# Kernel optimization log

Hardware: AMD Instinct MI355X
Metric: run time of the kernel (lower is better)

The kernel has to match this reference:

```python
import jax, jax.numpy as jnp
import numpy as np

P = 2        # patch size (all 3 dims)
NB = 8       # num_bands
N = 16       # d_state
DTR = 8      # dt_rank = d_model // 16
DCONV = 4    # d_conv
SMAX = 2.0   # smax_dt = smax_B = smax_C


def _ln(x, g, b):
    mu = x.mean(-1, keepdims=True)
    v = ((x - mu) ** 2).mean(-1, keepdims=True)
    return (x - mu) / jnp.sqrt(v + 1e-5) * g + b


def _silu(x):
    return x * jax.nn.sigmoid(x)


def _ssm_layer(x, band, m, rho, Win, bin_, convw, convb, Wx, Wdt, bdt, Alog, Dp,
               Wout, bout, edt, eB, eC, wr, wm):
    # x: [B, L, d_model] -> bidirectional conditioned selective scan (BiFCSSM)
    Bsz, L, _ = x.shape
    ED = convw.shape[0]
    xz = x @ Win + bin_
    xp, z = xz[..., :ED], xz[..., ED:]
    # depthwise causal conv1d over L
    xpad = jnp.pad(xp, ((0, 0), (DCONV - 1, 0), (0, 0)))
    xc = sum(xpad[:, k:k + L, :] * convw[:, k] for k in range(DCONV)) + convb
    xc = _silu(xc)
    dbl = xc @ Wx                                    # [B,L,DTR+2N]
    dt = jax.nn.softplus(dbl[..., :DTR] @ Wdt + bdt)  # [B,L,ED]
    # band/radius/mask conditioned modulation of delta, B, C
    s_dt = SMAX * jax.nn.sigmoid(edt[band][None] + wr[0] * rho[None] + wm[0] * m)
    s_B = SMAX * jax.nn.sigmoid(eB[band][None] + wr[1] * rho[None] + wm[1] * m)
    s_C = SMAX * jax.nn.sigmoid(eC[band][None] + wr[2] * rho[None] + wm[2] * m)
    dt = dt * s_dt[..., None]
    Bm = dbl[..., DTR:DTR + N] * s_B[..., None]       # [B,L,N]
    Cm = dbl[..., DTR + N:] * s_C[..., None]          # [B,L,N]
    A = -jnp.exp(Alog)                                # [ED,N]
    dA = jnp.exp(dt[..., None] * A)                   # [B,L,ED,N]
    dBu = (dA - 1.0) / A * Bm[:, :, None, :] * xc[..., None]   # exact ZOH
    dA_s = jnp.moveaxis(dA, 1, 0)
    dBu_s = jnp.moveaxis(dBu, 1, 0)
    C_s = jnp.moveaxis(Cm, 1, 0)
    h0 = jnp.zeros((Bsz, ED, N), x.dtype)

    def step(h, inp):
        a, bu, c = inp
        h = a * h + bu
        return h, jnp.einsum('ben,bn->be', h, c)

    _, yf = jax.lax.scan(step, h0, (dA_s, dBu_s, C_s))
    _, yb = jax.lax.scan(step, h0, (dA_s, dBu_s, C_s), reverse=True)
    y = jnp.moveaxis(yf + yb, 0, 1) + Dp * xc
    y = y * _silu(z)
    return y @ Wout + bout


def _fwd(kspace_ri, mask, pe_w, pe_b, pu_w, pu_b, ln_g, ln_b, fn_g, fn_b,
         cond_band, cond_rad_w, cond_mask_w, l0_Win, l0_bin, l0_convw, l0_convb,
         l0_Wx, l0_Wdt, l0_bdt, l0_Alog, l0_D, l0_Wout, l0_bout, l0_edt, l0_eB,
         l0_eC, l0_wr, l0_wm):
    Bsz, C, nx, ny, nz = kspace_ri.shape
    gx, gy, gz = nx // P, ny // P, nz // P
    L = gx * gy * gz
    # patch embed (Conv3d, kernel==stride) as blocked einsum
    xr = kspace_ri.reshape(Bsz, C, gx, P, gy, P, gz, P)
    x = jnp.einsum('bcxiyjzk,dcijk->bdxyz', xr, pe_w) + pe_b[None, :, None, None, None]
    DM = x.shape[1]
    x = x.reshape(Bsz, DM, L).transpose(0, 2, 1)               # [B,L,D]
    m = mask.reshape(Bsz, 1, gx, P, gy, P, gz, P).mean(axis=(3, 5, 7)).reshape(Bsz, L)
    m = jnp.clip(m, 0.0, 1.0)
    # raster scan ordering: identity permutation, rho_bar, band ids
    rho = jnp.arange(L, dtype=x.dtype) / float(L - 1)
    band = jnp.clip(jnp.floor(rho * NB).astype(jnp.int32), 0, NB - 1)
    # condition tokens
    cond = cond_band[band][None] + rho[None, :, None] * cond_rad_w + m[:, :, None] * cond_mask_w
    h = _ln(x + cond, ln_g, ln_b)
    h = h + _ssm_layer(_ln(h, fn_g, fn_b), band, m, rho, l0_Win, l0_bin, l0_convw,
                       l0_convb, l0_Wx, l0_Wdt, l0_bdt, l0_Alog, l0_D, l0_Wout,
                       l0_bout, l0_edt, l0_eB, l0_eC, l0_wr, l0_wm)
    # patch unembed (ConvTranspose3d, kernel==stride) as blocked einsum
    hg = h.transpose(0, 2, 1).reshape(Bsz, DM, gx, gy, gz)
    out = jnp.einsum('bdxyz,dcijk->bcxiyjzk', hg, pu_w).reshape(Bsz, C, nx, ny, nz)
    out = out + pu_b[None, :, None, None, None]
    return kspace_ri + out


def setup_inputs() -> dict:
    key = jax.random.key(0)
    ks = jax.random.split(key, 24)
    ED, DM, CIN = 256, 128, 16

    def nrm(k, shape, s):
        return jax.random.normal(k, shape, jnp.float32) * s

    return {
        'kspace_ri': jax.random.normal(ks[0], (1, CIN, 64, 64, 16), jnp.float32),
        'mask': jax.random.uniform(ks[1], (1, 1, 64, 64, 16), jnp.float32),
        'pe_w': nrm(ks[2], (DM, CIN, P, P, P), 0.09),
        'pe_b': nrm(ks[3], (DM,), 0.02),
        'pu_w': nrm(ks[4], (DM, CIN, P, P, P), 0.05),
        'pu_b': jnp.zeros((CIN,), jnp.float32),
        'ln_g': jnp.ones((DM,), jnp.float32),
        'ln_b': jnp.zeros((DM,), jnp.float32),
        'fn_g': jnp.ones((DM,), jnp.float32),
        'fn_b': jnp.zeros((DM,), jnp.float32),
        'cond_band': nrm(ks[5], (NB, DM), 0.02),
        'cond_rad_w': nrm(ks[6], (DM,), 0.02),
        'cond_mask_w': nrm(ks[7], (DM,), 0.02),
        'l0_Win': nrm(ks[8], (DM, 2 * ED), 0.05),
        'l0_bin': jnp.zeros((2 * ED,), jnp.float32),
        'l0_convw': nrm(ks[9], (ED, DCONV), 0.2),
        'l0_convb': jnp.zeros((ED,), jnp.float32),
        'l0_Wx': nrm(ks[10], (ED, DTR + 2 * N), 0.05),
        'l0_Wdt': nrm(ks[11], (DTR, ED), 0.1),
        'l0_bdt': jnp.full((ED,), -3.0, jnp.float32),
        'l0_Alog': jnp.log(jnp.tile(jnp.arange(1, N + 1, dtype=jnp.float32), (ED, 1))),
        'l0_D': jnp.ones((ED,), jnp.float32),
        'l0_Wout': nrm(ks[12], (ED, DM), 0.05),
        'l0_bout': jnp.zeros((DM,), jnp.float32),
        'l0_edt': nrm(ks[13], (NB,), 0.1),
        'l0_eB': nrm(ks[14], (NB,), 0.1),
        'l0_eC': nrm(ks[15], (NB,), 0.1),
        'l0_wr': nrm(ks[16], (3,), 0.1),
        'l0_wm': nrm(ks[17], (3,), 0.1),
    }


def reference(kspace_ri, mask, pe_w, pe_b, pu_w, pu_b, ln_g, ln_b, fn_g, fn_b,
              cond_band, cond_rad_w, cond_mask_w, l0_Win, l0_bin, l0_convw,
              l0_convb, l0_Wx, l0_Wdt, l0_bdt, l0_Alog, l0_D, l0_Wout, l0_bout,
              l0_edt, l0_eB, l0_eC, l0_wr, l0_wm):
    return _fwd(kspace_ri, mask, pe_w, pe_b, pu_w, pu_b, ln_g, ln_b, fn_g, fn_b,
                cond_band, cond_rad_w, cond_mask_w, l0_Win, l0_bin, l0_convw,
                l0_convb, l0_Wx, l0_Wdt, l0_bdt, l0_Alog, l0_D, l0_Wout, l0_bout,
                l0_edt, l0_eB, l0_eC, l0_wr, l0_wm)
```

## Files before the change

kernel.cpp:

```cpp
#include <hip/hip_runtime.h>
#include <hip/hip_bf16.h>

#define L_TOK 8192
#define NCh 256
#define CLh 32
#define LOG2E 1.44269504088896f

typedef short bf16x8 __attribute__((ext_vector_type(8)));
typedef float f32x4 __attribute__((ext_vector_type(4)));

static __device__ __forceinline__ float nexp2(float x) {
#if __has_builtin(__builtin_amdgcn_exp2f)
    return __builtin_amdgcn_exp2f(x);
#else
    return exp2f(x);
#endif
}
static __device__ __forceinline__ float sigm(float x) {
    return 1.f / (1.f + nexp2(-x * LOG2E));
}

static __device__ __forceinline__ ushort f2bf(float x) {
    union { float f; uint u; } v; v.f = x;
    uint r = v.u + 0x7fffu + ((v.u >> 16) & 1u);
    return (ushort)(r >> 16);
}
static __device__ __forceinline__ float bf2f(ushort h) {
    union { float f; uint u; } v; v.u = ((uint)h) << 16;
    return v.f;
}
static __device__ __forceinline__ void f2hl(float x, ushort* hi, ushort* lo) {
    ushort h = f2bf(x);
    *hi = h;
    *lo = f2bf(x - bf2f(h));
}

#define W_PE   0
#define W_WIN  16384
#define W_WOUT 81920
#define W_PU   114688
#define W_PROJ 131072
#define W_TOT  212992

__global__ __launch_bounds__(256) void prep_k(const float* __restrict__ pe_w, const float* __restrict__ Win,
                                              const float* __restrict__ Wx, const float* __restrict__ Wdt,
                                              const float* __restrict__ Wout, const float* __restrict__ pu_w,
                                              const float* __restrict__ mask,
                                              ushort* __restrict__ wH, ushort* __restrict__ wL,
                                              float* __restrict__ mbuf) {
    int b = blockIdx.x;
    if (b >= 832) {
        int l = (b - 832) * 256 + threadIdx.x;
        int xg = l >> 8, yg = (l >> 3) & 31, zg = l & 7;
        float s = 0.f;
        for (int i2 = 0; i2 < 2; ++i2)
            for (int j2 = 0; j2 < 2; ++j2)
                for (int k2 = 0; k2 < 2; ++k2)
                    s += mask[(2 * xg + i2) * 1024 + (2 * yg + j2) * 16 + 2 * zg + k2];
        s *= 0.125f;
        mbuf[l] = fminf(fmaxf(s, 0.f), 1.f);
        return;
    }
    int i = b * 256 + threadIdx.x;
    float v;
    if (i < 16384) {
        v = pe_w[i];
    } else if (i < 81920) {
        int j = i - 16384; int n = j >> 7, k = j & 127;
        v = Win[k * 512 + n];
    } else if (i < 114688) {
        int j = i - 81920; int n = j >> 8, k = j & 255;
        v = Wout[k * 128 + n];
    } else if (i < 131072) {
        int j = i - 114688; int n = j >> 7, k = j & 127;
        v = pu_w[k * 128 + n];
    } else {
        int j = i - 131072; int n = j >> 8, k = j & 255;
        if (n < 256) {
            float s = 0.f;
#pragma unroll
            for (int r = 0; r < 8; ++r) s += Wx[k * 40 + r] * Wdt[r * 256 + n];
            v = s;
        } else if (n < 288) {
            v = Wx[k * 40 + 8 + (n - 256)];
        } else {
            v = 0.f;
        }
    }
    ushort h, lo; f2hl(v, &h, &lo);
    wH[i] = h; wL[i] = lo;
}

__global__ __launch_bounds__(256) void embed_ln_k(const float* __restrict__ ks,
                                                  const ushort* __restrict__ wH, const ushort* __restrict__ wL,
                                                  const float* __restrict__ pe_b, const float* __restrict__ cond_band,
                                                  const float* __restrict__ cond_rad, const float* __restrict__ cond_mask,
                                                  const float* __restrict__ mbuf,
                                                  const float* __restrict__ ln_g, const float* __restrict__ ln_b,
                                                  const float* __restrict__ fn_g, const float* __restrict__ fn_b,
                                                  float* __restrict__ h_,
                                                  ushort* __restrict__ hnH, ushort* __restrict__ hnL) {
    __shared__ __align__(16) char smem[41472];
    ushort (*AsH)[72] = (ushort(*)[72])(smem);
    ushort (*AsL)[72] = (ushort(*)[72])(smem + 2304);
    ushort (*BsH)[72] = (ushort(*)[72])(smem + 4608);
    ushort (*BsL)[72] = (ushort(*)[72])(smem + 23040);
    float  (*Cs)[132] = (float(*)[132])(smem);

    const int tid = threadIdx.x;
    const int lane = tid & 63, wn = tid >> 6;
    const int ln = lane & 15, q = lane >> 4;
    const int mb = blockIdx.x * 16;

    f32x4 acc[2];
    acc[0] = (f32x4){0.f, 0.f, 0.f, 0.f};
    acc[1] = (f32x4){0.f, 0.f, 0.f, 0.f};

    for (int kc = 0; kc < 128; kc += 64) {
        __syncthreads();
        for (int u = tid; u < 1024; u += 256) {
            int r = u >> 6, kk = u & 63;
            int l = mb + r, k = kc + kk;
            int cc = k >> 3, ijk = k & 7;
            int xg = l >> 8, yg = (l >> 3) & 31, zg = l & 7;
            int i2 = (ijk >> 2) & 1, j2 = (ijk >> 1) & 1, k2 = ijk & 1;
            float v = ks[cc * 65536 + (2 * xg + i2) * 1024 + (2 * yg + j2) * 16 + 2 * zg + k2];
            ushort h, lo; f2hl(v, &h, &lo);
            AsH[r][kk] = h; AsL[r][kk] = lo;
        }
        for (int u = tid; u < 1024; u += 256) {
            int n = u >> 3, g = u & 7;
            *(uint4*)&BsH[n][g * 8] = *(const uint4*)&wH[W_PE + n * 128 + kc + g * 8];
            *(uint4*)&BsL[n][g * 8] = *(const uint4*)&wL[W_PE + n * 128 + kc + g * 8];
        }
        __syncthreads();
#pragma unroll
        for (int ks_ = 0; ks_ < 64; ks_ += 32) {
            const int kk = ks_ + q * 8;
            bf16x8 ah = *(const bf16x8*)&AsH[ln][kk];
            bf16x8 al = *(const bf16x8*)&AsL[ln][kk];
#pragma unroll
            for (int cb = 0; cb < 2; ++cb) {
                bf16x8 bh = *(const bf16x8*)&BsH[wn * 32 + cb * 16 + ln][kk];
                bf16x8 bl = *(const bf16x8*)&BsL[wn * 32 + cb * 16 + ln][kk];
                acc[cb] = __builtin_amdgcn_mfma_f32_16x16x32_bf16(ah, bh, acc[cb], 0, 0, 0);
                acc[cb] = __builtin_amdgcn_mfma_f32_16x16x32_bf16(ah, bl, acc[cb], 0, 0, 0);
                acc[cb] = __builtin_amdgcn_mfma_f32_16x16x32_bf16(al, bh, acc[cb], 0, 0, 0);
            }
        }
    }
    __syncthreads();
#pragma unroll
    for (int cb = 0; cb < 2; ++cb) {
#pragma unroll
        for (int r = 0; r < 4; ++r) {
            int row = q * 4 + r;
            int col = wn * 32 + cb * 16 + ln;
            int l = mb + row;
            float rho = (float)l * (1.0f / 8191.0f);
            int band = min(7, (int)(rho * 8.0f));
            Cs[row][col] = acc[cb][r] + pe_b[col] + cond_band[band * 128 + col]
                           + rho * cond_rad[col] + mbuf[l] * cond_mask[col];
        }
    }
    __syncthreads();
    {
        int row = tid >> 4, j = tid & 15;
        int l = mb + row;
        float v8[8];
        float s = 0.f, s2 = 0.f;
#pragma unroll
        for (int i = 0; i < 8; ++i) {
            float v = Cs[row][j * 8 + i];
            v8[i] = v; s += v; s2 += v * v;
        }
#pragma unroll
        for (int o = 1; o < 16; o <<= 1) { s += __shfl_xor(s, o, 16); s2 += __shfl_xor(s2, o, 16); }
        float mu = s * (1.f / 128.f);
        float var = s2 * (1.f / 128.f) - mu * mu;
        float rstd = rsqrtf(fmaxf(var, 0.f) + 1e-5f);
        float hv[8];
        s = 0.f; s2 = 0.f;
#pragma unroll
        for (int i = 0; i < 8; ++i) {
            int col = j * 8 + i;
            float h = (v8[i] - mu) * rstd * ln_g[col] + ln_b[col];
            hv[i] = h; s += h; s2 += h * h;
        }
#pragma unroll
        for (int i = 0; i < 8; i += 4)
            *(float4*)&h_[(size_t)l * 128 + j * 8 + i] = make_float4(hv[i], hv[i + 1], hv[i + 2], hv[i + 3]);
#pragma unroll
        for (int o = 1; o < 16; o <<= 1) { s += __shfl_xor(s, o, 16); s2 += __shfl_xor(s2, o, 16); }
        mu = s * (1.f / 128.f);
        var = s2 * (1.f / 128.f) - mu * mu;
        rstd = rsqrtf(fmaxf(var, 0.f) + 1e-5f);
        union { ushort u[8]; uint4 v4; } oh, ol;
#pragma unroll
        for (int i = 0; i < 8; ++i) {
            int col = j * 8 + i;
            float o2 = (hv[i] - mu) * rstd * fn_g[col] + fn_b[col];
            ushort hh, ll; f2hl(o2, &hh, &ll);
            oh.u[i] = hh; ol.u[i] = ll;
        }
        *(uint4*)&hnH[(size_t)l * 128 + j * 8] = oh.v4;
        *(uint4*)&hnL[(size_t)l * 128 + j * 8] = ol.v4;
    }
}

__global__ __launch_bounds__(256) void win_k(const ushort* __restrict__ Ah, const ushort* __restrict__ Al,
                                             const ushort* __restrict__ wH, const ushort* __restrict__ wL,
                                             const float* __restrict__ bin_,
                                             float* __restrict__ xp, float* __restrict__ sz) {
    __shared__ ushort AsH[64][72], AsL[64][72];
    __shared__ ushort BsH[64][72], BsL[64][72];
    const int tid = threadIdx.x;
    const int lane = tid & 63, wave = tid >> 6;
    const int wm = wave & 1, wn = wave >> 1;
    const int ln = lane & 15, q = lane >> 4;
    const int mb = blockIdx.x * 64, nb = blockIdx.y * 64;

    f32x4 acc[2][2];
#pragma unroll
    for (int rb = 0; rb < 2; ++rb)
#pragma unroll
        for (int cb = 0; cb < 2; ++cb) acc[rb][cb] = (f32x4){0.f, 0.f, 0.f, 0.f};

    for (int kc = 0; kc < 128; kc += 64) {
        __syncthreads();
        for (int u = tid; u < 512; u += 256) {
            int r = u >> 3, g = u & 7;
            size_t go = (size_t)(mb + r) * 128 + kc + g * 8;
            *(uint4*)&AsH[r][g * 8] = *(const uint4*)&Ah[go];
            *(uint4*)&AsL[r][g * 8] = *(const uint4*)&Al[go];
        }
        for (int u = tid; u < 512; u += 256) {
            int n = u >> 3, g = u & 7;
            size_t go = (size_t)(W_WIN) + (size_t)(nb + n) * 128 + kc + g * 8;
            *(uint4*)&BsH[n][g * 8] = *(const uint4*)&wH[go];
            *(uint4*)&BsL[n][g * 8] = *(const uint4*)&wL[go];
        }
        __syncthreads();
#pragma unroll
        for (int ks_ = 0; ks_ < 64; ks_ += 32) {
            const int kk = ks_ + q * 8;
            bf16x8 ah[2], al[2], bh[2], bl[2];
#pragma unroll
            for (int rb = 0; rb < 2; ++rb) {
                ah[rb] = *(const bf16x8*)&AsH[wm * 32 + rb * 16 + ln][kk];
                al[rb] = *(const bf16x8*)&AsL[wm * 32 + rb * 16 + ln][kk];
            }
#pragma unroll
            for (int cb = 0; cb < 2; ++cb) {
                bh[cb] = *(const bf16x8*)&BsH[wn * 32 + cb * 16 + ln][kk];
                bl[cb] = *(const bf16x8*)&BsL[wn * 32 + cb * 16 + ln][kk];
            }
#pragma unroll
            for (int rb = 0; rb < 2; ++rb)
#pragma unroll
                for (int cb = 0; cb < 2; ++cb) {
                    acc[rb][cb] = __builtin_amdgcn_mfma_f32_16x16x32_bf16(ah[rb], bh[cb], acc[rb][cb], 0, 0, 0);
                    acc[rb][cb] = __builtin_amdgcn_mfma_f32_16x16x32_bf16(ah[rb], bl[cb], acc[rb][cb], 0, 0, 0);
                    acc[rb][cb] = __builtin_amdgcn_mfma_f32_16x16x32_bf16(al[rb], bh[cb], acc[rb][cb], 0, 0, 0);
                }
        }
    }
#pragma unroll
    for (int rb = 0; rb < 2; ++rb)
#pragma unroll
        for (int cb = 0; cb < 2; ++cb)
#pragma unroll
            for (int r = 0; r < 4; ++r) {
                int l = mb + wm * 32 + rb * 16 + q * 4 + r;
                int col = nb + wn * 32 + cb * 16 + ln;
                float v = acc[rb][cb][r] + bin_[col];
                if (col < 256) {
                    xp[(size_t)l * 256 + col] = v;
                } else {
                    sz[(size_t)l * 256 + (col - 256)] = v * sigm(v);
                }
            }
}

__global__ __launch_bounds__(256) void conv_k(const float* __restrict__ xp, const float* __restrict__ convw,
                                              const float* __restrict__ convb, float* __restrict__ xc) {
    int id = blockIdx.x * 256 + threadIdx.x;
    int l = id >> 6, e4 = (id & 63) * 4;
    float4 cw[4];
#pragma unroll
    for (int j = 0; j < 4; ++j) cw[j] = *(const float4*)&convw[(e4 + j) * 4];
    float4 cb = *(const float4*)&convb[e4];
    float o[4] = {cb.x, cb.y, cb.z, cb.w};
#pragma unroll
    for (int k = 0; k < 4; ++k) {
        int lp = l - 3 + k;
        if (lp >= 0) {
            float4 t = *(const float4*)&xp[(size_t)lp * 256 + e4];
            o[0] += t.x * ((const float*)&cw[0])[k];
            o[1] += t.y * ((const float*)&cw[1])[k];
            o[2] += t.z * ((const float*)&cw[2])[k];
            o[3] += t.w * ((const float*)&cw[3])[k];
        }
    }
    float4 r;
    r.x = o[0] * sigm(o[0]);
    r.y = o[1] * sigm(o[1]);
    r.z = o[2] * sigm(o[2]);
    r.w = o[3] * sigm(o[3]);
    *(float4*)&xc[(size_t)l * 256 + e4] = r;
}

__global__ __launch_bounds__(256) void proj_k(const float* __restrict__ xc,
                                              const ushort* __restrict__ wH, const ushort* __restrict__ wL,
                                              const float* __restrict__ bdt, const float* __restrict__ mbuf,
                                              const float* __restrict__ edt, const float* __restrict__ eB,
                                              const float* __restrict__ eC, const float* __restrict__ wr,
                                              const float* __restrict__ wm,
                                              float* __restrict__ dt, float* __restrict__ Bm, float* __restrict__ Cm) {
    __shared__ ushort AsH[64][72], AsL[64][72];
    __shared__ ushort BsH[64][72], BsL[64][72];
    const int tid = threadIdx.x;
    const int lane = tid & 63, wave = tid >> 6;
    const int wm_ = wave & 1, wn = wave >> 1;
    const int ln = lane & 15, q = lane >> 4;
    const int mb = blockIdx.x * 64, nb = blockIdx.y * 64;

    f32x4 acc[2][2];
#pragma unroll
    for (int rb = 0; rb < 2; ++rb)
#pragma unroll
        for (int cb = 0; cb < 2; ++cb) acc[rb][cb] = (f32x4){0.f, 0.f, 0.f, 0.f};

    for (int kc = 0; kc < 256; kc += 64) {
        __syncthreads();
        for (int u = tid; u < 1024; u += 256) {
            int r = u >> 4, kq = u & 15;
            float4 v = *(const float4*)&xc[(size_t)(mb + r) * 256 + kc + kq * 4];
            union { ushort u[4]; uint2 v2; } hh, ll;
            f2hl(v.x, &hh.u[0], &ll.u[0]); f2hl(v.y, &hh.u[1], &ll.u[1]);
            f2hl(v.z, &hh.u[2], &ll.u[2]); f2hl(v.w, &hh.u[3], &ll.u[3]);
            *(uint2*)&AsH[r][kq * 4] = hh.v2;
            *(uint2*)&AsL[r][kq * 4] = ll.v2;
        }
        for (int u = tid; u < 512; u += 256) {
            int n = u >> 3, g = u & 7;
            size_t go = (size_t)(W_PROJ) + (size_t)(nb + n) * 256 + kc + g * 8;
            *(uint4*)&BsH[n][g * 8] = *(const uint4*)&wH[go];
            *(uint4*)&BsL[n][g * 8] = *(const uint4*)&wL[go];
        }
        __syncthreads();
#pragma unroll
        for (int ks_ = 0; ks_ < 64; ks_ += 32) {
            const int kk = ks_ + q * 8;
            bf16x8 ah[2], al[2], bh[2], bl[2];
#pragma unroll
            for (int rb = 0; rb < 2; ++rb) {
                ah[rb] = *(const bf16x8*)&AsH[wm_ * 32 + rb * 16 + ln][kk];
                al[rb] = *(const bf16x8*)&AsL[wm_ * 32 + rb * 16 + ln][kk];
            }
#pragma unroll
            for (int cb = 0; cb < 2; ++cb) {
                bh[cb] = *(const bf16x8*)&BsH[wn * 32 + cb * 16 + ln][kk];
                bl[cb] = *(const bf16x8*)&BsL[wn * 32 + cb * 16 + ln][kk];
            }
#pragma unroll
            for (int rb = 0; rb < 2; ++rb)
#pragma unroll
                for (int cb = 0; cb < 2; ++cb) {
                    acc[rb][cb] = __builtin_amdgcn_mfma_f32_16x16x32_bf16(ah[rb], bh[cb], acc[rb][cb], 0, 0, 0);
                    acc[rb][cb] = __builtin_amdgcn_mfma_f32_16x16x32_bf16(ah[rb], bl[cb], acc[rb][cb], 0, 0, 0);
                    acc[rb][cb] = __builtin_amdgcn_mfma_f32_16x16x32_bf16(al[rb], bh[cb], acc[rb][cb], 0, 0, 0);
                }
        }
    }
#pragma unroll
    for (int rb = 0; rb < 2; ++rb)
#pragma unroll
        for (int cb = 0; cb < 2; ++cb)
#pragma unroll
            for (int r = 0; r < 4; ++r) {
                int l = mb + wm_ * 32 + rb * 16 + q * 4 + r;
                int col = nb + wn * 32 + cb * 16 + ln;
                float v = acc[rb][cb][r];
                float rho = (float)l * (1.0f / 8191.0f);
                int band = min(7, (int)(rho * 8.0f));
                float mv = mbuf[l];
                if (col < 256) {
                    float sc0 = 2.0f * sigm(edt[band] + wr[0] * rho + wm[0] * mv);
                    float v2 = v + bdt[col];
                    float sp = (v2 > 20.f) ? v2 : log1pf(expf(v2));
                    dt[(size_t)l * 256 + col] = sp * sc0;
                } else if (col < 272) {
                    float sc1 = 2.0f * sigm(eB[band] + wr[1] * rho + wm[1] * mv);
                    Bm[(size_t)l * 16 + (col - 256)] = v * sc1;
                } else if (col < 288) {
                    float sc2 = 2.0f * sigm(eC[band] + wr[2] * rho + wm[2] * mv);
                    Cm[(size_t)l * 16 + (col - 272)] = v * sc2;
                }
            }
}

template <int PHASE>
__global__ __launch_bounds__(256) void scan_k(const float* __restrict__ dt, const float* __restrict__ xc,
                                              const float* __restrict__ Bm, const float* __restrict__ Cm,
                                              const float* __restrict__ Alog,
                                              float* __restrict__ Hb, float* __restrict__ sdtb,
                                              float* __restrict__ yf, float* __restrict__ yb) {
    const int c = blockIdx.x, dir = blockIdx.y, e = threadIdx.x;
    __shared__ float bms[CLh][16];
    __shared__ float cms[CLh][16];
    for (int idx = e; idx < CLh * 16; idx += 256) {
        bms[idx >> 4][idx & 15] = Bm[c * (CLh * 16) + idx];
        if (PHASE == 1) cms[idx >> 4][idx & 15] = Cm[c * (CLh * 16) + idx];
    }
    float A2[16], iv[16], h[16];
#pragma unroll
    for (int n = 0; n < 16; ++n) {
        float ea = nexp2(Alog[e * 16 + n] * LOG2E);
        A2[n] = -ea * LOG2E;
        iv[n] = -1.0f / ea;
    }
    const size_t hofs = (size_t)(dir * NCh + c) * 4096 + e * 16;
    if (PHASE == 0) {
#pragma unroll
        for (int n = 0; n < 16; ++n) h[n] = 0.f;
    } else {
#pragma unroll
        for (int j = 0; j < 4; ++j) {
            float4 hv = *(const float4*)&Hb[hofs + 4 * j];
            h[4 * j] = hv.x; h[4 * j + 1] = hv.y; h[4 * j + 2] = hv.z; h[4 * j + 3] = hv.w;
        }
    }
    const int base = c * CLh;
    float cu[8], cx[8], nu[8], nx[8];
#pragma unroll
    for (int j = 0; j < 8; ++j) {
        int p = dir ? (CLh - 1 - j) : j;
        cu[j] = dt[(size_t)(base + p) * 256 + e];
        cx[j] = xc[(size_t)(base + p) * 256 + e];
    }
    __syncthreads();
    float sdt = 0.f;
    float* __restrict__ yp = dir ? yb : yf;
#pragma unroll
    for (int g = 0; g < CLh / 8; ++g) {
        if (g + 1 < CLh / 8) {
#pragma unroll
            for (int j = 0; j < 8; ++j) {
                int s = (g + 1) * 8 + j;
                int p = dir ? (CLh - 1 - s) : s;
                nu[j] = dt[(size_t)(base + p) * 256 + e];
                nx[j] = xc[(size_t)(base + p) * 256 + e];
            }
        }
#pragma unroll
        for (int j = 0; j < 8; ++j) {
            int s = g * 8 + j;
            int p = dir ? (CLh - 1 - s) : s;
            float u = cu[j], xv = cx[j];
            union { float4 v[4]; float f[16]; } bb, cc;
            const float4* bp = (const float4*)&bms[p][0];
            bb.v[0] = bp[0]; bb.v[1] = bp[1]; bb.v[2] = bp[2]; bb.v[3] = bp[3];
            if (PHASE == 1) {
                const float4* cp = (const float4*)&cms[p][0];
                cc.v[0] = cp[0]; cc.v[1] = cp[1]; cc.v[2] = cp[2]; cc.v[3] = cp[3];
            }
            float y = 0.f;
#pragma unroll
            for (int n = 0; n < 16; ++n) {
                float a = nexp2(A2[n] * u);
                float w = xv * bb.f[n] * iv[n];
                float t = h[n] + w;
                h[n] = a * t - w;
                if (PHASE == 1) y += h[n] * cc.f[n];
            }
            if (PHASE == 0) sdt += u;
            if (PHASE == 1) yp[(size_t)(base + p) * 256 + e] = y;
        }
#pragma unroll
        for (int j = 0; j < 8; ++j) { cu[j] = nu[j]; cx[j] = nx[j]; }
    }
    if (PHASE == 0) {
#pragma unroll
        for (int j = 0; j < 4; ++j) {
            float4 hv = make_float4(h[4 * j], h[4 * j + 1], h[4 * j + 2], h[4 * j + 3]);
            *(float4*)&Hb[hofs + 4 * j] = hv;
        }
        if (dir == 0) sdtb[c * 256 + e] = sdt;
    }
}

__global__ __launch_bounds__(64) void combine_k(const float* __restrict__ Hb, float* __restrict__ Hpre,
                                                const float* __restrict__ sdtb, const float* __restrict__ Alog) {
    int id = blockIdx.x * 64 + threadIdx.x;
    int dir = id >> 12, en = id & 4095, e = en >> 4;
    float A2 = -nexp2(Alog[en] * LOG2E) * LOG2E;
    float hi = 0.f;
    for (int g = 0; g < NCh / 8; ++g) {
        float Pv[8], qv[8];
#pragma unroll
        for (int j = 0; j < 8; ++j) {
            int c = dir ? (NCh - 1 - (g * 8 + j)) : (g * 8 + j);
            Pv[j] = sdtb[c * 256 + e];
            qv[j] = Hb[(size_t)(dir * NCh + c) * 4096 + en];
        }
#pragma unroll
        for (int j = 0; j < 8; ++j) {
            int c = dir ? (NCh - 1 - (g * 8 + j)) : (g * 8 + j);
            float P = nexp2(A2 * Pv[j]);
            Hpre[(size_t)(dir * NCh + c) * 4096 + en] = hi;
            hi = P * hi + qv[j];
        }
    }
}

__global__ __launch_bounds__(256) void wout_k(const float* __restrict__ yf, const float* __restrict__ yb,
                                              const float* __restrict__ xc, const float* __restrict__ sz,
                                              const float* __restrict__ Dp,
                                              const ushort* __restrict__ wH, const ushort* __restrict__ wL,
                                              const float* __restrict__ bout, const float* __restrict__ h_,
                                              ushort* __restrict__ hfH, ushort* __restrict__ hfL) {
    __shared__ ushort AsH[32][72], AsL[32][72];
    __shared__ ushort BsH[64][72], BsL[64][72];
    const int tid = threadIdx.x;
    const int lane = tid & 63, wave = tid >> 6;
    const int wm = wave & 1, wn = wave >> 1;
    const int ln = lane & 15, q = lane >> 4;
    const int mb = blockIdx.x * 32, nb = blockIdx.y * 64;

    f32x4 acc[2];
    acc[0] = (f32x4){0.f, 0.f, 0.f, 0.f};
    acc[1] = (f32x4){0.f, 0.f, 0.f, 0.f};

    for (int kc = 0; kc < 256; kc += 64) {
        __syncthreads();
        for (int u = tid; u < 512; u += 256) {
            int r = u >> 4, kq = u & 15;
            size_t go = (size_t)(mb + r) * 256 + kc + kq * 4;
            float4 a = *(const float4*)&yf[go];
            float4 b = *(const float4*)&yb[go];
            float4 x = *(const float4*)&xc[go];
            float4 s = *(const float4*)&sz[go];
            float4 d = *(const float4*)&Dp[kc + kq * 4];
            float v0 = (a.x + b.x + d.x * x.x) * s.x;
            float v1 = (a.y + b.y + d.y * x.y) * s.y;
            float v2 = (a.z + b.z + d.z * x.z) * s.z;
            float v3 = (a.w + b.w + d.w * x.w) * s.w;
            union { ushort u[4]; uint2 v2; } hh, ll;
            f2hl(v0, &hh.u[0], &ll.u[0]); f2hl(v1, &hh.u[1], &ll.u[1]);
            f2hl(v2, &hh.u[2], &ll.u[2]); f2hl(v3, &hh.u[3], &ll.u[3]);
            *(uint2*)&AsH[r][kq * 4] = hh.v2;
            *(uint2*)&AsL[r][kq * 4] = ll.v2;
        }
        for (int u = tid; u < 512; u += 256) {
            int n = u >> 3, g = u & 7;
            size_t go = (size_t)(W_WOUT) + (size_t)(nb + n) * 256 + kc + g * 8;
            *(uint4*)&BsH[n][g * 8] = *(const uint4*)&wH[go];
            *(uint4*)&BsL[n][g * 8] = *(const uint4*)&wL[go];
        }
        __syncthreads();
#pragma unroll
        for (int ks_ = 0; ks_ < 64; ks_ += 32) {
            const int kk = ks_ + q * 8;
            bf16x8 ah = *(const bf16x8*)&AsH[wm * 16 + ln][kk];
            bf16x8 al = *(const bf16x8*)&AsL[wm * 16 + ln][kk];
#pragma unroll
            for (int cb = 0; cb < 2; ++cb) {
                bf16x8 bh = *(const bf16x8*)&BsH[wn * 32 + cb * 16 + ln][kk];
                bf16x8 bl = *(const bf16x8*)&BsL[wn * 32 + cb * 16 + ln][kk];
                acc[cb] = __builtin_amdgcn_mfma_f32_16x16x32_bf16(ah, bh, acc[cb], 0, 0, 0);
                acc[cb] = __builtin_amdgcn_mfma_f32_16x16x32_bf16(ah, bl, acc[cb], 0, 0, 0);
                acc[cb] = __builtin_amdgcn_mfma_f32_16x16x32_bf16(al, bh, acc[cb], 0, 0, 0);
            }
        }
    }
#pragma unroll
    for (int cb = 0; cb < 2; ++cb)
#pragma unroll
        for (int r = 0; r < 4; ++r) {
            int l = mb + wm * 16 + q * 4 + r;
            int col = nb + wn * 32 + cb * 16 + ln;
            float v = acc[cb][r] + bout[col] + h_[(size_t)l * 128 + col];
            ushort hh, ll; f2hl(v, &hh, &ll);
            hfH[(size_t)l * 128 + col] = hh;
            hfL[(size_t)l * 128 + col] = ll;
        }
}

__global__ __launch_bounds__(256) void unembed_k(const ushort* __restrict__ Ah, const ushort* __restrict__ Al,
                                                 const ushort* __restrict__ wH, const ushort* __restrict__ wL,
                                                 const float* __restrict__ pu_b, const float* __restrict__ ks,
                                                 float* __restrict__ out) {
    __shared__ ushort AsH[32][72], AsL[32][72];
    __shared__ ushort BsH[64][72], BsL[64][72];
    const int tid = threadIdx.x;
    const int lane = tid & 63, wave = tid >> 6;
    const int wm = wave & 1, wn = wave >> 1;
    const int ln = lane & 15, q = lane >> 4;
    const int mb = blockIdx.x * 32, nb = blockIdx.y * 64;

    f32x4 acc[2];
    acc[0] = (f32x4){0.f, 0.f, 0.f, 0.f};
    acc[1] = (f32x4){0.f, 0.f, 0.f, 0.f};

    for (int kc = 0; kc < 128; kc += 64) {
        __syncthreads();
        for (int u = tid; u < 256; u += 256) {
            int r = u >> 3, g = u & 7;
            size_t go = (size_t)(mb + r) * 128 + kc + g * 8;
            *(uint4*)&AsH[r][g * 8] = *(const uint4*)&Ah[go];
            *(uint4*)&AsL[r][g * 8] = *(const uint4*)&Al[go];
        }
        for (int u = tid; u < 512; u += 256) {
            int n = u >> 3, g = u & 7;
            size_t go = (size_t)(W_PU) + (size_t)(nb + n) * 128 + kc + g * 8;
            *(uint4*)&BsH[n][g * 8] = *(const uint4*)&wH[go];
            *(uint4*)&BsL[n][g * 8] = *(const uint4*)&wL[go];
        }
        __syncthreads();
#pragma unroll
        for (int ks_ = 0; ks_ < 64; ks_ += 32) {
            const int kk = ks_ + q * 8;
            bf16x8 ah = *(const bf16x8*)&AsH[wm * 16 + ln][kk];
            bf16x8 al = *(const bf16x8*)&AsL[wm * 16 + ln][kk];
#pragma unroll
            for (int cb = 0; cb < 2; ++cb) {
                bf16x8 bh = *(const bf16x8*)&BsH[wn * 32 + cb * 16 + ln][kk];
                bf16x8 bl = *(const bf16x8*)&BsL[wn * 32 + cb * 16 + ln][kk];
                acc[cb] = __builtin_amdgcn_mfma_f32_16x16x32_bf16(ah, bh, acc[cb], 0, 0, 0);
                acc[cb] = __builtin_amdgcn_mfma_f32_16x16x32_bf16(ah, bl, acc[cb], 0, 0, 0);
                acc[cb] = __builtin_amdgcn_mfma_f32_16x16x32_bf16(al, bh, acc[cb], 0, 0, 0);
            }
        }
    }
#pragma unroll
    for (int cb = 0; cb < 2; ++cb)
#pragma unroll
        for (int r = 0; r < 4; ++r) {
            int l = mb + wm * 16 + q * 4 + r;
            int col = nb + wn * 32 + cb * 16 + ln;
            int xg = l >> 8, yg = (l >> 3) & 31, zg = l & 7;
            int c = col >> 3, ijk = col & 7;
            int i2 = (ijk >> 2) & 1, j2 = (ijk >> 1) & 1, k2 = ijk & 1;
            size_t idx = (size_t)((c * 64 + 2 * xg + i2) * 64 + (2 * yg + j2)) * 16 + 2 * zg + k2;
            out[idx] = acc[cb][r] + pu_b[c] + ks[idx];
        }
}

extern "C" void kernel_launch(void* const* d_in, const int* in_sizes, int n_in,
                              void* d_out, int out_size, void* d_ws, size_t ws_size,
                              hipStream_t stream) {
    const float* ks    = (const float*)d_in[0];
    const float* mask  = (const float*)d_in[1];
    const float* pe_w  = (const float*)d_in[2];
    const float* pe_b  = (const float*)d_in[3];
    const float* pu_w  = (const float*)d_in[4];
    const float* pu_b  = (const float*)d_in[5];
    const float* ln_g  = (const float*)d_in[6];
    const float* ln_b  = (const float*)d_in[7];
    const float* fn_g  = (const float*)d_in[8];
    const float* fn_b  = (const float*)d_in[9];
    const float* cond_band = (const float*)d_in[10];
    const float* cond_rad  = (const float*)d_in[11];
    const float* cond_mask = (const float*)d_in[12];
    const float* Win   = (const float*)d_in[13];
    const float* bin_  = (const float*)d_in[14];
    const float* convw = (const float*)d_in[15];
    const float* convb = (const float*)d_in[16];
    const float* Wx    = (const float*)d_in[17];
    const float* Wdt   = (const float*)d_in[18];
    const float* bdt   = (const float*)d_in[19];
    const float* Alog  = (const float*)d_in[20];
    const float* Dp    = (const float*)d_in[21];
    const float* Wout  = (const float*)d_in[22];
    const float* bout  = (const float*)d_in[23];
    const float* edt   = (const float*)d_in[24];
    const float* eB    = (const float*)d_in[25];
    const float* eC    = (const float*)d_in[26];
    const float* wr    = (const float*)d_in[27];
    const float* wm    = (const float*)d_in[28];
    float* out = (float*)d_out;

    char* base = (char*)d_ws;
    size_t o = 0;
    auto alloc = [&](size_t bytes) { char* p = base + o; o += (bytes + 255) & ~(size_t)255; return p; };
    float*  mbuf = (float*)alloc(32768);
    ushort* wH   = (ushort*)alloc(W_TOT * 2);
    ushort* wL   = (ushort*)alloc(W_TOT * 2);
    float*  h_   = (float*)alloc(4194304);
    ushort* hnH  = (ushort*)alloc(2097152);
    ushort* hnL  = (ushort*)alloc(2097152);
    float*  xp   = (float*)alloc(8388608);
    float*  sz   = (float*)alloc(8388608);
    float*  xc   = (float*)alloc(8388608);
    float*  dt   = (float*)alloc(8388608);
    float*  Bm   = (float*)alloc(524288);
    float*  Cm   = (float*)alloc(524288);
    float*  Hb   = (float*)alloc(8388608);
    float*  Hpre = (float*)alloc(8388608);
    float*  sdtb = (float*)alloc(262144);
    float*  yf   = (float*)alloc(8388608);
    float*  yb   = (float*)alloc(8388608);
    ushort* hfH  = (ushort*)alloc(2097152);
    ushort* hfL  = (ushort*)alloc(2097152);

    prep_k<<<864, 256, 0, stream>>>(pe_w, Win, Wx, Wdt, Wout, pu_w, mask, wH, wL, mbuf);
    embed_ln_k<<<512, 256, 0, stream>>>(ks, wH, wL, pe_b, cond_band, cond_rad, cond_mask, mbuf,
                                        ln_g, ln_b, fn_g, fn_b, h_, hnH, hnL);
    win_k<<<dim3(128, 8), 256, 0, stream>>>(hnH, hnL, wH, wL, bin_, xp, sz);
    conv_k<<<2048, 256, 0, stream>>>(xp, convw, convb, xc);
    proj_k<<<dim3(128, 5), 256, 0, stream>>>(xc, wH, wL, bdt, mbuf, edt, eB, eC, wr, wm, dt, Bm, Cm);
    scan_k<0><<<dim3(NCh, 2), 256, 0, stream>>>(dt, xc, Bm, Cm, Alog, Hb, sdtb, nullptr, nullptr);
    combine_k<<<128, 64, 0, stream>>>(Hb, Hpre, sdtb, Alog);
    scan_k<1><<<dim3(NCh, 2), 256, 0, stream>>>(dt, xc, Bm, Cm, Alog, Hpre, sdtb, yf, yb);
    wout_k<<<dim3(256, 2), 256, 0, stream>>>(yf, yb, xc, sz, Dp, wH, wL, bout, h_, hfH, hfL);
    unembed_k<<<dim3(256, 2), 256, 0, stream>>>(hfH, hfL, wH, wL, pu_b, ks, out);
}
```

Measured before the change: 239.9 us.

## Fuse both scan directions and output gating into one scan kernel

```diff
diff --git a/kernel.cpp b/kernel.cpp
--- a/kernel.cpp
+++ b/kernel.cpp
@@ -19,7 +19,6 @@
 static __device__ __forceinline__ float sigm(float x) {
     return 1.f / (1.f + nexp2(-x * LOG2E));
 }
-
 static __device__ __forceinline__ ushort f2bf(float x) {
     union { float f; uint u; } v; v.f = x;
     uint r = v.u + 0x7fffu + ((v.u >> 16) & 1u);
@@ -400,36 +399,20 @@
             }
 }
 
-template <int PHASE>
-__global__ __launch_bounds__(256) void scan_k(const float* __restrict__ dt, const float* __restrict__ xc,
-                                              const float* __restrict__ Bm, const float* __restrict__ Cm,
-                                              const float* __restrict__ Alog,
-                                              float* __restrict__ Hb, float* __restrict__ sdtb,
-                                              float* __restrict__ yf, float* __restrict__ yb) {
+__global__ __launch_bounds__(256) void scan0_k(const float* __restrict__ dt, const float* __restrict__ xc,
+                                               const float* __restrict__ Bm, const float* __restrict__ Alog,
+                                               float* __restrict__ Hb, float* __restrict__ sdtb) {
     const int c = blockIdx.x, dir = blockIdx.y, e = threadIdx.x;
     __shared__ float bms[CLh][16];
-    __shared__ float cms[CLh][16];
-    for (int idx = e; idx < CLh * 16; idx += 256) {
+    for (int idx = e; idx < CLh * 16; idx += 256)
         bms[idx >> 4][idx & 15] = Bm[c * (CLh * 16) + idx];
-        if (PHASE == 1) cms[idx >> 4][idx & 15] = Cm[c * (CLh * 16) + idx];
-    }
     float A2[16], iv[16], h[16];
 #pragma unroll
     for (int n = 0; n < 16; ++n) {
         float ea = nexp2(Alog[e * 16 + n] * LOG2E);
         A2[n] = -ea * LOG2E;
         iv[n] = -1.0f / ea;
-    }
-    const size_t hofs = (size_t)(dir * NCh + c) * 4096 + e * 16;
-    if (PHASE == 0) {
-#pragma unroll
-        for (int n = 0; n < 16; ++n) h[n] = 0.f;
-    } else {
-#pragma unroll
-        for (int j = 0; j < 4; ++j) {
-            float4 hv = *(const float4*)&Hb[hofs + 4 * j];
-            h[4 * j] = hv.x; h[4 * j + 1] = hv.y; h[4 * j + 2] = hv.z; h[4 * j + 3] = hv.w;
-        }
+        h[n] = 0.f;
     }
     const int base = c * CLh;
     float cu[8], cx[8], nu[8], nx[8];
@@ -441,7 +424,6 @@
     }
     __syncthreads();
     float sdt = 0.f;
-    float* __restrict__ yp = dir ? yb : yf;
 #pragma unroll
     for (int g = 0; g < CLh / 8; ++g) {
         if (g + 1 < CLh / 8) {
@@ -458,36 +440,25 @@
             int s = g * 8 + j;
             int p = dir ? (CLh - 1 - s) : s;
             float u = cu[j], xv = cx[j];
-            union { float4 v[4]; float f[16]; } bb, cc;
+            union { float4 v[4]; float f[16]; } bb;
             const float4* bp = (const float4*)&bms[p][0];
             bb.v[0] = bp[0]; bb.v[1] = bp[1]; bb.v[2] = bp[2]; bb.v[3] = bp[3];
-            if (PHASE == 1) {
-                const float4* cp = (const float4*)&cms[p][0];
-                cc.v[0] = cp[0]; cc.v[1] = cp[1]; cc.v[2] = cp[2]; cc.v[3] = cp[3];
-            }
-            float y = 0.f;
 #pragma unroll
             for (int n = 0; n < 16; ++n) {
                 float a = nexp2(A2[n] * u);
                 float w = xv * bb.f[n] * iv[n];
-                float t = h[n] + w;
-                h[n] = a * t - w;
-                if (PHASE == 1) y += h[n] * cc.f[n];
-            }
-            if (PHASE == 0) sdt += u;
-            if (PHASE == 1) yp[(size_t)(base + p) * 256 + e] = y;
+                h[n] = a * (h[n] + w) - w;
+            }
+            sdt += u;
         }
 #pragma unroll
         for (int j = 0; j < 8; ++j) { cu[j] = nu[j]; cx[j] = nx[j]; }
     }
-    if (PHASE == 0) {
-#pragma unroll
-        for (int j = 0; j < 4; ++j) {
-            float4 hv = make_float4(h[4 * j], h[4 * j + 1], h[4 * j + 2], h[4 * j + 3]);
-            *(float4*)&Hb[hofs + 4 * j] = hv;
-        }
-        if (dir == 0) sdtb[c * 256 + e] = sdt;
-    }
+    const size_t hofs = (size_t)(dir * NCh + c) * 4096 + e * 16;
+#pragma unroll
+    for (int j = 0; j < 4; ++j)
+        *(float4*)&Hb[hofs + 4 * j] = make_float4(h[4 * j], h[4 * j + 1], h[4 * j + 2], h[4 * j + 3]);
+    if (dir == 0) sdtb[c * 256 + e] = sdt;
 }
 
 __global__ __launch_bounds__(64) void combine_k(const float* __restrict__ Hb, float* __restrict__ Hpre,
@@ -514,9 +485,98 @@
     }
 }
 
-__global__ __launch_bounds__(256) void wout_k(const float* __restrict__ yf, const float* __restrict__ yb,
-                                              const float* __restrict__ xc, const float* __restrict__ sz,
-                                              const float* __restrict__ Dp,
+__global__ __launch_bounds__(512) void scan1g_k(const float* __restrict__ dt, const float* __restrict__ xc,
+                                                const float* __restrict__ Bm, const float* __restrict__ Cm,
+                                                const float* __restrict__ Alog, const float* __restrict__ Hpre,
+                                                const float* __restrict__ sz, const float* __restrict__ Dp,
+                                                ushort* __restrict__ AHo, ushort* __restrict__ ALo) {
+    const int c = blockIdx.x;
+    const int tid = threadIdx.x;
+    const int dir = tid >> 8;
+    const int e = tid & 255;
+    __shared__ float bms[CLh][16];
+    __shared__ float cms[CLh][16];
+    __shared__ float ysum[CLh][256];
+    for (int idx = tid; idx < CLh * 16; idx += 512) {
+        bms[idx >> 4][idx & 15] = Bm[c * (CLh * 16) + idx];
+        cms[idx >> 4][idx & 15] = Cm[c * (CLh * 16) + idx];
+    }
+    float A2[16], iv[16], h[16];
+#pragma unroll
+    for (int n = 0; n < 16; ++n) {
+        float ea = nexp2(Alog[e * 16 + n] * LOG2E);
+        A2[n] = -ea * LOG2E;
+        iv[n] = -1.0f / ea;
+    }
+    const size_t hofs = (size_t)(dir * NCh + c) * 4096 + e * 16;
+#pragma unroll
+    for (int j = 0; j < 4; ++j) {
+        float4 hv = *(const float4*)&Hpre[hofs + 4 * j];
+        h[4 * j] = hv.x; h[4 * j + 1] = hv.y; h[4 * j + 2] = hv.z; h[4 * j + 3] = hv.w;
+    }
+    const int base = c * CLh;
+    float yreg[CLh];
+    float cu[8], cx[8], nu[8], nx[8];
+#pragma unroll
+    for (int j = 0; j < 8; ++j) {
+        int p = dir ? (CLh - 1 - j) : j;
+        cu[j] = dt[(size_t)(base + p) * 256 + e];
+        cx[j] = xc[(size_t)(base + p) * 256 + e];
+    }
+    __syncthreads();
+#pragma unroll
+    for (int g = 0; g < CLh / 8; ++g) {
+        if (g + 1 < CLh / 8) {
+#pragma unroll
+            for (int j = 0; j < 8; ++j) {
+                int s = (g + 1) * 8 + j;
+                int p = dir ? (CLh - 1 - s) : s;
+                nu[j] = dt[(size_t)(base + p) * 256 + e];
+                nx[j] = xc[(size_t)(base + p) * 256 + e];
+            }
+        }
+#pragma unroll
+        for (int j = 0; j < 8; ++j) {
+            int s = g * 8 + j;
+            int p = dir ? (CLh - 1 - s) : s;
+            float u = cu[j], xv = cx[j];
+            union { float4 v[4]; float f[16]; } bb, cc;
+            const float4* bp = (const float4*)&bms[p][0];
+            bb.v[0] = bp[0]; bb.v[1] = bp[1]; bb.v[2] = bp[2]; bb.v[3] = bp[3];
+            const float4* cp = (const float4*)&cms[p][0];
+            cc.v[0] = cp[0]; cc.v[1] = cp[1]; cc.v[2] = cp[2]; cc.v[3] = cp[3];
+            float y = 0.f;
+#pragma unroll
+            for (int n = 0; n < 16; ++n) {
+                float a = nexp2(A2[n] * u);
+                float w = xv * bb.f[n] * iv[n];
+                h[n] = a * (h[n] + w) - w;
+                y += h[n] * cc.f[n];
+            }
+            yreg[p] = y;
+        }
+#pragma unroll
+        for (int j = 0; j < 8; ++j) { cu[j] = nu[j]; cx[j] = nx[j]; }
+    }
+    __syncthreads();
+    if (dir == 0) {
+#pragma unroll
+        for (int l = 0; l < CLh; ++l) ysum[l][e] = yreg[l];
+    }
+    __syncthreads();
+    if (dir == 1) {
+        float dpv = Dp[e];
+#pragma unroll
+        for (int l = 0; l < CLh; ++l) {
+            size_t gl = (size_t)(base + l) * 256 + e;
+            float a = (ysum[l][e] + yreg[l] + dpv * xc[gl]) * sz[gl];
+            ushort hh, ll; f2hl(a, &hh, &ll);
+            AHo[gl] = hh; ALo[gl] = ll;
+        }
+    }
+}
+
+__global__ __launch_bounds__(256) void wout_k(const ushort* __restrict__ AH, const ushort* __restrict__ AL,
                                               const ushort* __restrict__ wH, const ushort* __restrict__ wL,
                                               const float* __restrict__ bout, const float* __restrict__ h_,
                                               ushort* __restrict__ hfH, ushort* __restrict__ hfL) {
@@ -534,23 +594,11 @@
 
     for (int kc = 0; kc < 256; kc += 64) {
         __syncthreads();
-        for (int u = tid; u < 512; u += 256) {
-            int r = u >> 4, kq = u & 15;
-            size_t go = (size_t)(mb + r) * 256 + kc + kq * 4;
-            float4 a = *(const float4*)&yf[go];
-            float4 b = *(const float4*)&yb[go];
-            float4 x = *(const float4*)&xc[go];
-            float4 s = *(const float4*)&sz[go];
-            float4 d = *(const float4*)&Dp[kc + kq * 4];
-            float v0 = (a.x + b.x + d.x * x.x) * s.x;
-            float v1 = (a.y + b.y + d.y * x.y) * s.y;
-            float v2 = (a.z + b.z + d.z * x.z) * s.z;
-            float v3 = (a.w + b.w + d.w * x.w) * s.w;
-            union { ushort u[4]; uint2 v2; } hh, ll;
-            f2hl(v0, &hh.u[0], &ll.u[0]); f2hl(v1, &hh.u[1], &ll.u[1]);
-            f2hl(v2, &hh.u[2], &ll.u[2]); f2hl(v3, &hh.u[3], &ll.u[3]);
-            *(uint2*)&AsH[r][kq * 4] = hh.v2;
-            *(uint2*)&AsL[r][kq * 4] = ll.v2;
+        for (int u = tid; u < 256; u += 256) {
+            int r = u >> 3, g = u & 7;
+            size_t go = (size_t)(mb + r) * 256 + kc + g * 8;
+            *(uint4*)&AsH[r][g * 8] = *(const uint4*)&AH[go];
+            *(uint4*)&AsL[r][g * 8] = *(const uint4*)&AL[go];
         }
         for (int u = tid; u < 512; u += 256) {
             int n = u >> 3, g = u & 7;
@@ -699,8 +747,8 @@
     float*  Hb   = (float*)alloc(8388608);
     float*  Hpre = (float*)alloc(8388608);
     float*  sdtb = (float*)alloc(262144);
-    float*  yf   = (float*)alloc(8388608);
-    float*  yb   = (float*)alloc(8388608);
+    ushort* AHo  = (ushort*)alloc(4194304);
+    ushort* ALo  = (ushort*)alloc(4194304);
     ushort* hfH  = (ushort*)alloc(2097152);
     ushort* hfL  = (ushort*)alloc(2097152);
 
@@ -710,9 +758,9 @@
     win_k<<<dim3(128, 8), 256, 0, stream>>>(hnH, hnL, wH, wL, bin_, xp, sz);
     conv_k<<<2048, 256, 0, stream>>>(xp, convw, convb, xc);
     proj_k<<<dim3(128, 5), 256, 0, stream>>>(xc, wH, wL, bdt, mbuf, edt, eB, eC, wr, wm, dt, Bm, Cm);
-    scan_k<0><<<dim3(NCh, 2), 256, 0, stream>>>(dt, xc, Bm, Cm, Alog, Hb, sdtb, nullptr, nullptr);
+    scan0_k<<<dim3(NCh, 2), 256, 0, stream>>>(dt, xc, Bm, Alog, Hb, sdtb);
     combine_k<<<128, 64, 0, stream>>>(Hb, Hpre, sdtb, Alog);
-    scan_k<1><<<dim3(NCh, 2), 256, 0, stream>>>(dt, xc, Bm, Cm, Alog, Hpre, sdtb, yf, yb);
-    wout_k<<<dim3(256, 2), 256, 0, stream>>>(yf, yb, xc, sz, Dp, wH, wL, bout, h_, hfH, hfL);
+    scan1g_k<<<NCh, 512, 0, stream>>>(dt, xc, Bm, Cm, Alog, Hpre, sz, Dp, AHo, ALo);
+    wout_k<<<dim3(256, 2), 256, 0, stream>>>(AHo, ALo, wH, wL, bout, h_, hfH, hfL);
     unembed_k<<<dim3(256, 2), 256, 0, stream>>>(hfH, hfL, wH, wL, pu_b, ks, out);
 }
```

Measured after the change: 368.4 us. 53.5% more time.
